# Optimization experiments

Measured on AMD Instinct MI355X. Metric: run time of the kernel, lower is better.

## Reference

```python
import jax, jax.numpy as jnp
import numpy as np

N_QUBITS = 8
N_PAIRS = 4
PAIRS = [(2 * p, 2 * p + 1) for p in range(N_PAIRS)]
STRENGTH = 0.8
DIM = 2 ** N_QUBITS


def _apply_1q_full(st, G, q):
    # st: (2,)*n complex64 state, G: [2,2] gate on qubit q (qubit 0 = most significant)
    out = jnp.tensordot(G, st, axes=([1], [q]))
    return jnp.moveaxis(out, 0, q)


def _apply_ctrl_full(st, G, c, t):
    # controlled-G: apply G on target axis t only where control axis c == 1
    s0 = jnp.take(st, 0, axis=c)
    s1 = jnp.take(st, 1, axis=c)
    t2 = t if t < c else t - 1
    s1 = jnp.moveaxis(jnp.tensordot(G, s1, axes=([1], [t2])), 0, t2)
    return jnp.stack([s0, s1], axis=c)


def _entangled_base():
    # |0...0> -> H on q1, partial CNOT (controlled-RX(pi*strength)) on (q1,q2) per pair
    st = jnp.zeros((2,) * N_QUBITS, jnp.complex64).at[(0,) * N_QUBITS].set(1.0)
    H = jnp.array([[1.0, 1.0], [1.0, -1.0]], jnp.complex64) / np.float32(np.sqrt(2.0))
    th = np.float32(np.pi * STRENGTH)
    c, s = np.float32(np.cos(th / 2)), np.float32(np.sin(th / 2))
    RX = jnp.array([[c, -1j * s], [-1j * s, c]], jnp.complex64)
    for q1, q2 in PAIRS:
        st = _apply_1q_full(st, H, q1)
        st = _apply_ctrl_full(st, RX, q1, q2)
    return st.reshape(-1)


def _rx(theta):
    # RX(theta) = [[cos t/2, -i sin t/2], [-i sin t/2, cos t/2]], batched over theta shape
    cz = jnp.cos(0.5 * theta).astype(jnp.complex64)
    sz = (-1j) * jnp.sin(0.5 * theta).astype(jnp.complex64)
    return jnp.stack([jnp.stack([cz, sz], -1), jnpp_stack_fix(sz, cz)], -2) if False else jnp.stack([jnp.stack([cz, sz], -1), jnp.stack([sz, cz], -1)], -2)


def _rz(theta):
    ph = (0.5j) * theta.astype(jnp.complex64)
    e0, e1 = jnp.exp(-ph), jnp.exp(ph)
    z = jnp.zeros_like(e0)
    return jnp.stack([jnp.stack([e0, z], -1), jnp.stack([z, e1], -1)], -2)


def _quantum_scores(k_states):
    # k_states: [B,S,2*n_qubits] -> expected pair-agreement score [B,S]
    B, S, _ = k_states.shape
    k = k_states.reshape(B, S, N_QUBITS, 2)
    eye = jnp.eye(2, dtype=jnp.complex64)
    st = jnp.broadcast_to(_entangled_base(), (B, S, DIM))  # fresh entangled register per (b,j)
    for q in range(N_QUBITS):
        th_x, th_z = k[:, :, q, 0], k[:, :, q, 1]
        Gx = jnp.where((th_x > 0)[..., None, None], _rx(th_x), eye)
        Gz = jnp.where((th_z > 0)[..., None, None], _rz(th_z), eye)
        G = jnp.einsum('bsij,bsjk->bsik', Gz, Gx)  # RX applied first, then RZ
        L = 2 ** q
        R = DIM // (2 * L)
        stv = st.reshape(B, S, L, 2, R)
        st = jnp.einsum('bsij,bsljr->bslir', G, stv).reshape(B, S, DIM)
    probs = (st.real ** 2 + st.imag ** 2).reshape((B, S) + (2,) * N_QUBITS)
    score = jnp.zeros((B, S), probs.dtype)
    for q1, q2 in PAIRS:
        axes = tuple(2 + a for a in range(N_QUBITS) if a not in (q1, q2))
        marg = probs.sum(axis=axes)  # [B,S,2,2] joint marginal of the pair
        score = score + marg[..., 0, 0] + marg[..., 1, 1]  # P(measure equal)
    return score / N_PAIRS


def reference(query, key, value, Wq, bq, Wk, bk, Wv, bv, Wo, bo):
    q_states = query @ Wq + bq  # computed as in original forward (unused by scores)
    k_states = key @ Wk + bk    # [B,S,2*n_qubits]
    v_states = value @ Wv + bv  # [B,S,d_model]
    B, S, _ = k_states.shape
    score = _quantum_scores(k_states)  # [B,S]; deterministic expected agreement
    # original loop makes score[b,i,j] independent of i under independent per-(b,i,j) sims
    attn = jnp.broadcast_to(score[:, None, :], (B, S, S))
    w = jax.nn.softmax(attn, axis=-1)
    out = jnp.einsum('bij,bjd->bid', w, v_states)
    return out @ Wo + bo


def setup_inputs() -> dict:
    rng = jax.random.key(0)
    ks = jax.random.split(rng, 8)
    B, S, D = 8, 2048, 512
    nq2 = 2 * N_QUBITS
    f = jax.random.normal
    return {
        'query': f(ks[0], (B, S, D), jnp.float32),
        'key': f(ks[1], (B, S, D), jnp.float32),
        'value': f(ks[2], (B, S, D), jnp.float32),
        'Wq': f(ks[3], (D, nq2), jnp.float32) * 0.05,
        'bq': jnp.zeros((nq2,), jnp.float32),
        'Wk': f(ks[4], (D, nq2), jnp.float32) * 0.05,
        'bk': jnp.zeros((nq2,), jnp.float32),
        'Wv': f(ks[5], (D, D), jnp.float32) * 0.05,
        'bv': jnp.zeros((D,), jnp.float32),
        'Wo': f(ks[6], (D, D), jnp.float32) * 0.05,
        'bo': jnp.zeros((D,), jnp.float32),
    }
```

## Files before the change

### kernel.cpp

```cpp
#include <hip/hip_runtime.h>
#include <math.h>

#define DEV __device__ __forceinline__

struct C2 { float x, y; };
DEV C2 cmul(C2 a, C2 b){ return {a.x*b.x - a.y*b.y, a.x*b.y + a.y*b.x}; }
DEV C2 cadd(C2 a, C2 b){ return {a.x+b.x, a.y+b.y}; }
DEV C2 cscale(C2 a, float s){ return {a.x*s, a.y*s}; }
DEV C2 cnegi(C2 a){ return {a.y, -a.x}; }

__global__ __launch_bounds__(512, 4) void k_score_wsum(const float* __restrict__ key,
                                                       const float* __restrict__ Wk,
                                                       const float* __restrict__ bk,
                                                       const float* __restrict__ value,
                                                       float* __restrict__ partial,
                                                       float* __restrict__ partialw)
{
    const int c = blockIdx.x;
    const int b = blockIdx.y;
    const int t = threadIdx.x;
    const int lane = t & 63;
    const int wv   = t >> 6;
    const int h    = wv & 1;
    const int pr   = wv >> 1;
    const int base = b * 2048 + c * 32;
    const int wrow0 = pr * 8;

    __shared__ float  kslds[2][32][16];
    __shared__ float4 red[8][128];
    __shared__ float  wsums[4];

    float4 wk[4][4];
    #pragma unroll
    for (int jj = 0; jj < 4; ++jj) {
        const float4* w0 = (const float4*)(Wk + (h * 256 + 4 * lane + jj) * 16);
        #pragma unroll
        for (int q = 0; q < 4; ++q) wk[jj][q] = w0[q];
    }
    const float c0 = 0.30901699437494745f;
    const float s0 = 0.9510565162951535f;

    const float4* kp = (const float4*)(key + (size_t)(base + wrow0) * 512);
    float4 cur = kp[h * 64 + lane];
    #pragma unroll
    for (int j = 0; j < 8; ++j) {
        float4 nx;
        if (j < 7) nx = kp[(j + 1) * 128 + h * 64 + lane];
        float el[4] = {cur.x, cur.y, cur.z, cur.w};
        float acc[16];
        #pragma unroll
        for (int k = 0; k < 16; ++k) acc[k] = 0.f;
        #pragma unroll
        for (int jj = 0; jj < 4; ++jj) {
            #pragma unroll
            for (int q = 0; q < 4; ++q) {
                acc[4*q+0] = fmaf(el[jj], wk[jj][q].x, acc[4*q+0]);
                acc[4*q+1] = fmaf(el[jj], wk[jj][q].y, acc[4*q+1]);
                acc[4*q+2] = fmaf(el[jj], wk[jj][q].z, acc[4*q+2]);
                acc[4*q+3] = fmaf(el[jj], wk[jj][q].w, acc[4*q+3]);
            }
        }
        #pragma unroll
        for (int s = 0; s < 4; ++s) {
            const int m = 1 << s;
            const int bbit = (lane >> s) & 1;
            #pragma unroll
            for (int jj = 0; jj < (16 >> (s + 1)); ++jj) {
                float send = bbit ? acc[2*jj] : acc[2*jj+1];
                float keep = bbit ? acc[2*jj+1] : acc[2*jj];
                acc[jj] = keep + __shfl_xor(send, m);
            }
        }
        float ks = acc[0];
        ks += __shfl_xor(ks, 16);
        ks += __shfl_xor(ks, 32);
        if (lane < 16) kslds[h][wrow0 + j][lane] = ks;
        cur = nx;
    }

    const int vrow0 = wrow0 + h * 4;
    const float4* vp = (const float4*)(value + (size_t)(base + vrow0) * 512);
    float4 vreg[8];
    #pragma unroll
    for (int j = 0; j < 4; ++j) {
        vreg[2*j]   = vp[j * 128 + lane];
        vreg[2*j+1] = vp[j * 128 + 64 + lane];
    }
    __syncthreads();

    const int p  = (lane >> 3) & 3;
    const int jr = lane & 7;
    float4 k0 = *(const float4*)&kslds[0][wrow0 + jr][4 * p];
    float4 k1 = *(const float4*)&kslds[1][wrow0 + jr][4 * p];
    float4 bk4 = ((const float4*)bk)[p];
    float ax = k0.x + k1.x + bk4.x, az = k0.y + k1.y + bk4.y;
    float bx = k0.z + k1.z + bk4.z, bz = k0.w + k1.w + bk4.w;
    float cxa = 1.f, sxa = 0.f; if (ax > 0.f){ sxa = __sinf(0.5f*ax); cxa = __cosf(0.5f*ax); }
    float cpa = 1.f, spa = 0.f; if (az > 0.f){ spa = __sinf(0.5f*az); cpa = __cosf(0.5f*az); }
    float cxb = 1.f, sxb = 0.f; if (bx > 0.f){ sxb = __sinf(0.5f*bx); cxb = __cosf(0.5f*bx); }
    float cpb = 1.f, spb = 0.f; if (bz > 0.f){ spb = __sinf(0.5f*bz); cpb = __cosf(0.5f*bz); }
    C2 A00{cpa*cxa, -spa*cxa}, A01{-spa*sxa, -cpa*sxa};
    C2 A10{spa*sxa, -cpa*sxa}, A11{ cpa*cxa,  spa*cxa};
    C2 B00{cpb*cxb, -spb*cxb}, B01{-spb*sxb, -cpb*sxb};
    C2 B10{spb*sxb, -cpb*sxb}, B11{ cpb*cxb,  spb*cxb};
    C2 u = cadd(cmul(B00, cadd(A00, cscale(A01, c0))),
                cscale(cnegi(cmul(A01, B01)), s0));
    C2 v = cadd(cmul(B10, cadd(A10, cscale(A11, c0))),
                cscale(cnegi(cmul(A11, B11)), s0));
    float ps = u.x*u.x + u.y*u.y + v.x*v.x + v.y*v.y;
    ps += __shfl_xor(ps, 8);
    ps += __shfl_xor(ps, 16);
    float w_all = __expf(ps * 0.125f);

    if (h == 0) {
        float sw = w_all;
        sw += __shfl_xor(sw, 1); sw += __shfl_xor(sw, 2); sw += __shfl_xor(sw, 4);
        if (lane == 0) wsums[pr] = sw;
    }

    float4 aA = {0.f,0.f,0.f,0.f}, aB = {0.f,0.f,0.f,0.f};
    #pragma unroll
    for (int j = 0; j < 4; ++j) {
        float wj = __shfl(w_all, h * 4 + j);
        float4 v0 = vreg[2*j], v1 = vreg[2*j+1];
        aA.x = fmaf(wj, v0.x, aA.x); aA.y = fmaf(wj, v0.y, aA.y);
        aA.z = fmaf(wj, v0.z, aA.z); aA.w = fmaf(wj, v0.w, aA.w);
        aB.x = fmaf(wj, v1.x, aB.x); aB.y = fmaf(wj, v1.y, aB.y);
        aB.z = fmaf(wj, v1.z, aB.z); aB.w = fmaf(wj, v1.w, aB.w);
    }
    red[wv][lane] = aA;
    red[wv][64 + lane] = aB;
    __syncthreads();
    if (t < 128) {
        float4 q0 = red[0][t], q1 = red[1][t], q2 = red[2][t], q3 = red[3][t];
        float4 q4 = red[4][t], q5 = red[5][t], q6 = red[6][t], q7 = red[7][t];
        float4 o = { q0.x+q1.x+q2.x+q3.x+q4.x+q5.x+q6.x+q7.x,
                     q0.y+q1.y+q2.y+q3.y+q4.y+q5.y+q6.y+q7.y,
                     q0.z+q1.z+q2.z+q3.z+q4.z+q5.z+q6.z+q7.z,
                     q0.w+q1.w+q2.w+q3.w+q4.w+q5.w+q6.w+q7.w };
        ((float4*)partial)[((size_t)b * 64 + c) * 128 + t] = o;
    }
    if (t == 0)
        partialw[b * 64 + c] = wsums[0] + wsums[1] + wsums[2] + wsums[3];
}

__global__ __launch_bounds__(512) void k_mid(const float* __restrict__ partial,
                                             const float* __restrict__ partialw,
                                             const float* __restrict__ Wv,
                                             const float* __restrict__ bv,
                                             const float* __restrict__ Wo,
                                             const float* __restrict__ bo,
                                             float* __restrict__ frow)
{
    const int dt = blockIdx.x;
    const int b  = blockIdx.y;
    const int t  = threadIdx.x;

    __shared__ float cbuf[512];
    __shared__ float xbuf[512];
    __shared__ float red[512];
    __shared__ float sS;

    if (t < 64) {
        float s = partialw[b * 64 + t];
        s += __shfl_xor(s, 1);  s += __shfl_xor(s, 2);
        s += __shfl_xor(s, 4);  s += __shfl_xor(s, 8);
        s += __shfl_xor(s, 16); s += __shfl_xor(s, 32);
        if (t == 0) sS = 1.f / s;
    }

    {
        float c0 = 0.f, c1 = 0.f, c2 = 0.f, c3 = 0.f;
        const float* pp = partial + (size_t)b * 32768 + t;
        #pragma unroll
        for (int cc = 0; cc < 64; cc += 4) {
            c0 += pp[(size_t)cc * 512];
            c1 += pp[(size_t)(cc + 1) * 512];
            c2 += pp[(size_t)(cc + 2) * 512];
            c3 += pp[(size_t)(cc + 3) * 512];
        }
        cbuf[t] = (c0 + c1) + (c2 + c3);
    }
    __syncthreads();
    const float invS = sS;

    {
        float a0=0.f,a1=0.f,a2=0.f,a3=0.f,a4=0.f,a5=0.f,a6=0.f,a7=0.f;
        #pragma unroll 8
        for (int e = 0; e < 512; e += 8) {
            a0 = fmaf(cbuf[e],   Wv[(size_t)e * 512 + t],     a0);
            a1 = fmaf(cbuf[e+1], Wv[(size_t)(e+1) * 512 + t], a1);
            a2 = fmaf(cbuf[e+2], Wv[(size_t)(e+2) * 512 + t], a2);
            a3 = fmaf(cbuf[e+3], Wv[(size_t)(e+3) * 512 + t], a3);
            a4 = fmaf(cbuf[e+4], Wv[(size_t)(e+4) * 512 + t], a4);
            a5 = fmaf(cbuf[e+5], Wv[(size_t)(e+5) * 512 + t], a5);
            a6 = fmaf(cbuf[e+6], Wv[(size_t)(e+6) * 512 + t], a6);
            a7 = fmaf(cbuf[e+7], Wv[(size_t)(e+7) * 512 + t], a7);
        }
        xbuf[t] = (((a0+a1)+(a2+a3)) + ((a4+a5)+(a6+a7))) * invS + bv[t];
    }
    __syncthreads();

    {
        const int dl = t & 63, g = t >> 6;
        const int d  = dt * 64 + dl;
        const float* Wc = Wo + (size_t)(g * 64) * 512 + d;
        const float* xg = xbuf + g * 64;
        float a0=0.f,a1=0.f,a2=0.f,a3=0.f;
        #pragma unroll 8
        for (int e = 0; e < 64; e += 4) {
            a0 = fmaf(xg[e],   Wc[(size_t)e * 512],       a0);
            a1 = fmaf(xg[e+1], Wc[(size_t)(e+1) * 512],   a1);
            a2 = fmaf(xg[e+2], Wc[(size_t)(e+2) * 512],   a2);
            a3 = fmaf(xg[e+3], Wc[(size_t)(e+3) * 512],   a3);
        }
        red[t] = (a0 + a1) + (a2 + a3);
    }
    __syncthreads();
    if (t < 64) {
        float r = red[t]       + red[t + 64]  + red[t + 128] + red[t + 192]
                + red[t + 256] + red[t + 320] + red[t + 384] + red[t + 448];
        frow[b * 512 + dt * 64 + t] = r + bo[dt * 64 + t];
    }
}

__global__ __launch_bounds__(256) void k_bcast(const float* __restrict__ frow,
                                               float* __restrict__ out)
{
    int s = blockIdx.x, b = blockIdx.y, t = threadIdx.x;
    const int col4 = t & 127, h = t >> 7;
    float4 val = ((const float4*)frow)[b * 128 + col4];
    float4* o4 = (float4*)out
               + ((size_t)b * 2048 + s * 32 + h * 16) * 128 + col4;
    #pragma unroll
    for (int r = 0; r < 16; ++r) o4[(size_t)r * 128] = val;
}

extern "C" void kernel_launch(void* const* d_in, const int* in_sizes, int n_in,
                              void* d_out, int out_size, void* d_ws, size_t ws_size,
                              hipStream_t stream) {
    const float* key   = (const float*)d_in[1];
    const float* value = (const float*)d_in[2];
    const float* Wk    = (const float*)d_in[5];
    const float* bk    = (const float*)d_in[6];
    const float* Wv    = (const float*)d_in[7];
    const float* bv    = (const float*)d_in[8];
    const float* Wo    = (const float*)d_in[9];
    const float* bo    = (const float*)d_in[10];
    float* out = (float*)d_out;
    float* ws  = (float*)d_ws;

    float* partial  = ws;
    float* partialw = ws + 262144;
    float* frow     = ws + 262656;

    k_score_wsum<<<dim3(64, 8), 512, 0, stream>>>(key, Wk, bk, value,
                                                  partial, partialw);
    k_mid       <<<dim3(8, 8),  512, 0, stream>>>(partial, partialw,
                                                  Wv, bv, Wo, bo, frow);
    k_bcast     <<<dim3(64, 8), 256, 0, stream>>>(frow, out);
}
```

Before: 168.8 us.

## Shrink score kernel blocks to 128 threads, 8 rows each, quadruple grid

The score/weighted-sum kernel now uses 2-wave blocks covering 8 rows instead of 8-wave blocks covering 32 rows, giving 2048 blocks instead of 512. Value loads are issued before the key projection so they overlap with it. The per-block partial sums and weight sums grow fourfold, and the mid kernel now reduces 256 partials per batch instead of 64. This trades more block-level parallelism and finer scheduling for extra partial-buffer traffic and a longer reduction in k_mid.

Result: slower. 182.0 us (+7.8%).

```diff
diff --git a/kernel.cpp b/kernel.cpp
--- a/kernel.cpp
+++ b/kernel.cpp
@@ -9,7 +9,7 @@
 DEV C2 cscale(C2 a, float s){ return {a.x*s, a.y*s}; }
 DEV C2 cnegi(C2 a){ return {a.y, -a.x}; }
 
-__global__ __launch_bounds__(512, 4) void k_score_wsum(const float* __restrict__ key,
+__global__ __launch_bounds__(128, 4) void k_score_wsum(const float* __restrict__ key,
                                                        const float* __restrict__ Wk,
                                                        const float* __restrict__ bk,
                                                        const float* __restrict__ value,
@@ -20,15 +20,11 @@
     const int b = blockIdx.y;
     const int t = threadIdx.x;
     const int lane = t & 63;
-    const int wv   = t >> 6;
-    const int h    = wv & 1;
-    const int pr   = wv >> 1;
-    const int base = b * 2048 + c * 32;
-    const int wrow0 = pr * 8;
-
-    __shared__ float  kslds[2][32][16];
-    __shared__ float4 red[8][128];
-    __shared__ float  wsums[4];
+    const int h    = t >> 6;
+    const int base = b * 2048 + c * 8;
+
+    __shared__ float  kslds[2][8][16];
+    __shared__ float4 red[2][128];
 
     float4 wk[4][4];
     #pragma unroll
@@ -37,10 +33,19 @@
         #pragma unroll
         for (int q = 0; q < 4; ++q) wk[jj][q] = w0[q];
     }
+
+    const float4* vp = (const float4*)(value + (size_t)(base + h * 4) * 512);
+    float4 vreg[8];
+    #pragma unroll
+    for (int j = 0; j < 4; ++j) {
+        vreg[2*j]   = vp[j * 128 + lane];
+        vreg[2*j+1] = vp[j * 128 + 64 + lane];
+    }
+
     const float c0 = 0.30901699437494745f;
     const float s0 = 0.9510565162951535f;
 
-    const float4* kp = (const float4*)(key + (size_t)(base + wrow0) * 512);
+    const float4* kp = (const float4*)(key + (size_t)base * 512);
     float4 cur = kp[h * 64 + lane];
     #pragma unroll
     for (int j = 0; j < 8; ++j) {
@@ -74,24 +79,15 @@
         float ks = acc[0];
         ks += __shfl_xor(ks, 16);
         ks += __shfl_xor(ks, 32);
-        if (lane < 16) kslds[h][wrow0 + j][lane] = ks;
+        if (lane < 16) kslds[h][j][lane] = ks;
         cur = nx;
-    }
-
-    const int vrow0 = wrow0 + h * 4;
-    const float4* vp = (const float4*)(value + (size_t)(base + vrow0) * 512);
-    float4 vreg[8];
-    #pragma unroll
-    for (int j = 0; j < 4; ++j) {
-        vreg[2*j]   = vp[j * 128 + lane];
-        vreg[2*j+1] = vp[j * 128 + 64 + lane];
     }
     __syncthreads();
 
     const int p  = (lane >> 3) & 3;
     const int jr = lane & 7;
-    float4 k0 = *(const float4*)&kslds[0][wrow0 + jr][4 * p];
-    float4 k1 = *(const float4*)&kslds[1][wrow0 + jr][4 * p];
+    float4 k0 = *(const float4*)&kslds[0][jr][4 * p];
+    float4 k1 = *(const float4*)&kslds[1][jr][4 * p];
     float4 bk4 = ((const float4*)bk)[p];
     float ax = k0.x + k1.x + bk4.x, az = k0.y + k1.y + bk4.y;
     float bx = k0.z + k1.z + bk4.z, bz = k0.w + k1.w + bk4.w;
@@ -115,7 +111,7 @@
     if (h == 0) {
         float sw = w_all;
         sw += __shfl_xor(sw, 1); sw += __shfl_xor(sw, 2); sw += __shfl_xor(sw, 4);
-        if (lane == 0) wsums[pr] = sw;
+        if (lane == 0) partialw[b * 256 + c] = sw;
     }
 
     float4 aA = {0.f,0.f,0.f,0.f}, aB = {0.f,0.f,0.f,0.f};
@@ -128,20 +124,14 @@
         aB.x = fmaf(wj, v1.x, aB.x); aB.y = fmaf(wj, v1.y, aB.y);
         aB.z = fmaf(wj, v1.z, aB.z); aB.w = fmaf(wj, v1.w, aB.w);
     }
-    red[wv][lane] = aA;
-    red[wv][64 + lane] = aB;
-    __syncthreads();
-    if (t < 128) {
-        float4 q0 = red[0][t], q1 = red[1][t], q2 = red[2][t], q3 = red[3][t];
-        float4 q4 = red[4][t], q5 = red[5][t], q6 = red[6][t], q7 = red[7][t];
-        float4 o = { q0.x+q1.x+q2.x+q3.x+q4.x+q5.x+q6.x+q7.x,
-                     q0.y+q1.y+q2.y+q3.y+q4.y+q5.y+q6.y+q7.y,
-                     q0.z+q1.z+q2.z+q3.z+q4.z+q5.z+q6.z+q7.z,
-                     q0.w+q1.w+q2.w+q3.w+q4.w+q5.w+q6.w+q7.w };
-        ((float4*)partial)[((size_t)b * 64 + c) * 128 + t] = o;
-    }
-    if (t == 0)
-        partialw[b * 64 + c] = wsums[0] + wsums[1] + wsums[2] + wsums[3];
+    red[h][lane]      = aA;
+    red[h][64 + lane] = aB;
+    __syncthreads();
+    {
+        float4 q0 = red[0][t], q1 = red[1][t];
+        float4 o = { q0.x+q1.x, q0.y+q1.y, q0.z+q1.z, q0.w+q1.w };
+        ((float4*)partial)[((size_t)b * 256 + c) * 128 + t] = o;
+    }
 }
 
 __global__ __launch_bounds__(512) void k_mid(const float* __restrict__ partial,
@@ -162,7 +152,8 @@
     __shared__ float sS;
 
     if (t < 64) {
-        float s = partialw[b * 64 + t];
+        const float* pw = partialw + b * 256;
+        float s = pw[t] + pw[64 + t] + pw[128 + t] + pw[192 + t];
         s += __shfl_xor(s, 1);  s += __shfl_xor(s, 2);
         s += __shfl_xor(s, 4);  s += __shfl_xor(s, 8);
         s += __shfl_xor(s, 16); s += __shfl_xor(s, 32);
@@ -171,9 +162,9 @@
 
     {
         float c0 = 0.f, c1 = 0.f, c2 = 0.f, c3 = 0.f;
-        const float* pp = partial + (size_t)b * 32768 + t;
-        #pragma unroll
-        for (int cc = 0; cc < 64; cc += 4) {
+        const float* pp = partial + (size_t)b * 131072 + t;
+        #pragma unroll 8
+        for (int cc = 0; cc < 256; cc += 4) {
             c0 += pp[(size_t)cc * 512];
             c1 += pp[(size_t)(cc + 1) * 512];
             c2 += pp[(size_t)(cc + 2) * 512];
@@ -251,11 +242,11 @@
     float* ws  = (float*)d_ws;
 
     float* partial  = ws;
-    float* partialw = ws + 262144;
-    float* frow     = ws + 262656;
-
-    k_score_wsum<<<dim3(64, 8), 512, 0, stream>>>(key, Wk, bk, value,
-                                                  partial, partialw);
+    float* partialw = ws + 1048576;
+    float* frow     = ws + 1050624;
+
+    k_score_wsum<<<dim3(256, 8), 128, 0, stream>>>(key, Wk, bk, value,
+                                                   partial, partialw);
     k_mid       <<<dim3(8, 8),  512, 0, stream>>>(partial, partialw,
                                                   Wv, bv, Wo, bo, frow);
     k_bcast     <<<dim3(64, 8), 256, 0, stream>>>(frow, out);
```
